# Kernel optimization log

Measured on AMD Instinct MI355X. Metric: run time of the kernel, lower is better.

The kernel has to match this reference:

```python
import jax, jax.numpy as jnp
import numpy as np

B, T, C = 4, 2048, 1024
H = 16
D = C // H  # head_dim = 64
SCALE = D ** -0.5


def setup_inputs() -> dict:
    key = jax.random.key(0)
    ks = jax.random.split(key, 5)
    x = jax.random.normal(ks[0], (B, T, C), dtype=jnp.float32)
    w_qkv = jax.random.normal(ks[1], (3 * C, C), dtype=jnp.float32) * (C ** -0.5)
    b_qkv = jnp.zeros((3 * C,), dtype=jnp.float32)
    w_proj = jax.random.normal(ks[2], (C, C), dtype=jnp.float32) * (C ** -0.5)
    b_proj = jnp.zeros((C,), dtype=jnp.float32)
    return {"x": x, "w_qkv": w_qkv, "b_qkv": b_qkv, "w_proj": w_proj, "b_proj": b_proj}


def reference(x, w_qkv, b_qkv, w_proj, b_proj):
    b, t, c = x.shape
    # fused qkv projection (torch Linear: x @ W.T + b)
    qkv = x @ w_qkv.T + b_qkv                      # [B, T, 3C]
    q, k, v = jnp.split(qkv, 3, axis=2)
    # [B, T, C] -> [B, H, T, D]
    q = q.reshape(b, t, H, D).transpose(0, 2, 1, 3)
    k = k.reshape(b, t, H, D).transpose(0, 2, 1, 3)
    v = v.reshape(b, t, H, D).transpose(0, 2, 1, 3)
    att = jnp.einsum('bhqd,bhkd->bhqk', q, k) * SCALE
    causal = jnp.tril(jnp.ones((t, t), dtype=bool))  # True = keep
    att = jnp.where(causal, att, -jnp.inf)
    att = jax.nn.softmax(att, axis=-1)
    out = jnp.einsum('bhqk,bhkd->bhqd', att, v)
    out = out.transpose(0, 2, 1, 3).reshape(b, t, c)
    return out @ w_proj.T + b_proj
```

## Files before the change

### kernel.cpp

```cpp
#include <hip/hip_runtime.h>

typedef unsigned short u16;
typedef __attribute__((ext_vector_type(8))) short short8;
typedef __attribute__((ext_vector_type(4))) float f32x4;
typedef __attribute__((ext_vector_type(16))) float f32x16;
typedef __attribute__((ext_vector_type(2))) unsigned uint2v;
typedef __attribute__((ext_vector_type(4))) unsigned u32x4;

#define AS1 __attribute__((address_space(1)))
#define AS3 __attribute__((address_space(3)))

constexpr int Bn = 4, Tn = 2048, Cn = 1024, Hn = 16, Dn = 64;
constexpr float SCL_LOG2E = 0.125f * 1.44269504088896f;

__device__ __forceinline__ u16 f2bf(float f) {
  union { float f; unsigned u; } v; v.f = f;
  unsigned r = v.u + 0x7FFFu + ((v.u >> 16) & 1u);
  return (u16)(r >> 16);
}

__device__ __forceinline__ unsigned cvtpk_bf16(float a, float b) {
  unsigned r;
  asm("v_cvt_pk_bf16_f32 %0, %1, %2" : "=v"(r) : "v"(a), "v"(b));
  return r;
}

__global__ void cast_f32_to_bf16(const float* __restrict__ in, u16* __restrict__ out, int n4) {
  int i = blockIdx.x * 256 + threadIdx.x;
  if (i >= n4) return;
  float4 v = ((const float4*)in)[i];
  ushort4 o;
  o.x = f2bf(v.x); o.y = f2bf(v.y); o.z = f2bf(v.z); o.w = f2bf(v.w);
  ((ushort4*)out)[i] = o;
}

template <typename OT>
__global__ __launch_bounds__(512) void gemm8(
    const u16* __restrict__ A, const u16* __restrict__ Bm,
    const float* __restrict__ bias, OT* __restrict__ C,
    int M, int N, int K, int nbn, int qcols, float qscale)
{
  __shared__ u16 As[2][128 * 64];
  __shared__ u16 Bs[2][128 * 64];

  const int tid = threadIdx.x;
  const int lane = tid & 63;
  const int w = tid >> 6;
  const int wm = w >> 2, wn = w & 3;
  const int l15 = lane & 15, lg = lane >> 4;

  const int nwg = gridDim.x;
  const int wg = (blockIdx.x & 7) * (nwg >> 3) + (blockIdx.x >> 3);
  const int m0 = (wg / nbn) * 128;
  const int n0 = (wg % nbn) * 128;
  const int NT = K >> 6;

  const int wrow = wm * 64;
  const int wcol = wn * 32;

  f32x4 acc[4][2] = {};

  auto stage_A = [&](int tt) {
    if (tt >= NT) return;
    const int bu = tt & 1;
#pragma unroll
    for (int it = 0; it < 2; ++it) {
      const int c = it * 512 + tid;
      const int row = c >> 3;
      const int cs = (c & 7) ^ (row & 7);
      const u16* g = A + (size_t)(m0 + row) * K + tt * 64 + cs * 8;
      __builtin_amdgcn_global_load_lds((const AS1 void*)g,
          (AS3 void*)(&As[bu][c * 8]), 16, 0, 0);
    }
  };
  auto stage_B = [&](int tt) {
    if (tt >= NT) return;
    const int bu = tt & 1;
#pragma unroll
    for (int it = 0; it < 2; ++it) {
      const int c = it * 512 + tid;
      const int row = c >> 3;
      const int cs = (c & 7) ^ (row & 7);
      const u16* g = Bm + (size_t)(n0 + row) * K + tt * 64 + cs * 8;
      __builtin_amdgcn_global_load_lds((const AS1 void*)g,
          (AS3 void*)(&Bs[bu][c * 8]), 16, 0, 0);
    }
  };

  auto readA = [&](int bu, int mh, short8 (*a)[2]) {
#pragma unroll
    for (int i = 0; i < 2; ++i)
#pragma unroll
      for (int ks = 0; ks < 2; ++ks) {
        const int ra = wrow + (mh * 2 + i) * 16 + l15;
        a[i][ks] = *(const short8*)(&As[bu][ra * 64 + (((ks * 4 + lg) ^ (ra & 7)) << 3)]);
      }
  };
  auto readB = [&](int bu, int nh, short8 (*b)[2]) {
#pragma unroll
    for (int ks = 0; ks < 2; ++ks) {
      const int rb = wcol + nh * 16 + l15;
      b[0][ks] = *(const short8*)(&Bs[bu][rb * 64 + (((ks * 4 + lg) ^ (rb & 7)) << 3)]);
    }
  };
  auto mmaq = [&](int mh, int nh, short8 (*a)[2], short8 (*b)[2]) {
    __builtin_amdgcn_s_setprio(1);
#pragma unroll
    for (int i = 0; i < 2; ++i)
#pragma unroll
      for (int ks = 0; ks < 2; ++ks)
        acc[mh * 2 + i][nh] = __builtin_amdgcn_mfma_f32_16x16x32_bf16(
            a[i][ks], b[0][ks], acc[mh * 2 + i][nh], 0, 0, 0);
    __builtin_amdgcn_s_setprio(0);
  };

  stage_A(0);
  stage_B(0);
  stage_A(1);
  asm volatile("s_waitcnt vmcnt(2)" ::: "memory");
  __builtin_amdgcn_sched_barrier(0);
  __builtin_amdgcn_s_barrier();

  for (int t = 0; t < NT; ++t) {
    const int bu = t & 1;
    short8 a0[2][2], a1[2][2], b0[1][2], b1[1][2];
    readA(bu, 0, a0);
    readB(bu, 0, b0);
    stage_B(t + 1);
    __builtin_amdgcn_s_barrier();
    mmaq(0, 0, a0, b0);
    __builtin_amdgcn_s_barrier();
    readB(bu, 1, b1);
    __builtin_amdgcn_s_barrier();
    mmaq(0, 1, a0, b1);
    __builtin_amdgcn_s_barrier();
    readA(bu, 1, a1);
    __builtin_amdgcn_s_barrier();
    mmaq(1, 1, a1, b1);
    __builtin_amdgcn_s_barrier();
    stage_A(t + 2);
    __builtin_amdgcn_s_barrier();
    mmaq(1, 0, a1, b0);
    if (t + 2 < NT) {
      asm volatile("s_waitcnt vmcnt(2)" ::: "memory");
      __builtin_amdgcn_sched_barrier(0);
    } else if (t + 1 < NT) {
      asm volatile("s_waitcnt vmcnt(0)" ::: "memory");
      __builtin_amdgcn_sched_barrier(0);
    }
    __builtin_amdgcn_s_barrier();
  }

  __syncthreads();
  if constexpr (__is_same(OT, u16)) {
    u16* bounce = &As[0][0];
#pragma unroll
    for (int i = 0; i < 4; ++i)
#pragma unroll
      for (int j = 0; j < 2; ++j) {
        const int colg = n0 + wcol + j * 16 + l15;
        const float sc = (colg < qcols) ? qscale : 1.0f;
        const float bv = bias[colg];
#pragma unroll
        for (int r = 0; r < 4; ++r)
          bounce[(wrow + i * 16 + lg * 4 + r) * 128 + wcol + j * 16 + l15] =
              f2bf((acc[i][j][r] + bv) * sc);
      }
    __syncthreads();
#pragma unroll
    for (int s = 0; s < 4; ++s) {
      const int u = s * 512 + tid;
      const int row = u >> 4, col = (u & 15) * 8;
      *(short8*)(C + (size_t)(m0 + row) * N + n0 + col) =
          *(const short8*)(&bounce[row * 128 + col]);
    }
  } else {
    float* bounce = (float*)&As[0][0];
#pragma unroll
    for (int cch = 0; cch < 2; ++cch) {
      if (wm == cch) {
#pragma unroll
        for (int i = 0; i < 4; ++i)
#pragma unroll
          for (int j = 0; j < 2; ++j) {
            const int colg = n0 + wcol + j * 16 + l15;
            const float bv = bias[colg];
#pragma unroll
            for (int r = 0; r < 4; ++r)
              bounce[(i * 16 + lg * 4 + r) * 128 + wcol + j * 16 + l15] =
                  acc[i][j][r] + bv;
          }
      }
      __syncthreads();
#pragma unroll
      for (int s = 0; s < 4; ++s) {
        const int u = s * 512 + tid;
        const int row = u >> 5, col = (u & 31) * 4;
        *(f32x4*)((float*)C + (size_t)(m0 + cch * 64 + row) * N + n0 + col) =
            *(const f32x4*)(&bounce[row * 128 + col]);
      }
      __syncthreads();
    }
  }
}

__global__ __launch_bounds__(256) void transpose_v(
    const u16* __restrict__ qkv, u16* __restrict__ vt)
{
  __shared__ u16 tile[64][72];
  const int bh = blockIdx.x >> 5;
  const int tt = blockIdx.x & 31;
  const int b = bh >> 4;
  const int h = bh & 15;
  const int tid = threadIdx.x;
  const int trow = tid >> 2;
  const int dseg = tid & 3;

  const u16* src = qkv + (size_t)(b * Tn + tt * 64 + trow) * (3 * Cn) + 2 * Cn + h * Dn + dseg * 16;
  short8 v0 = *(const short8*)src;
  short8 v1 = *(const short8*)(src + 8);
#pragma unroll
  for (int e = 0; e < 8; ++e) {
    tile[dseg * 16 + e][trow] = (u16)v0[e];
    tile[dseg * 16 + 8 + e][trow] = (u16)v1[e];
  }
  __syncthreads();

  const int drow = tid >> 2;
  const int tseg = tid & 3;
  u16* dst = vt + (size_t)(bh * Dn + drow) * Tn + tt * 64 + tseg * 16;
  *(short8*)dst = *(const short8*)&tile[drow][tseg * 16];
  *(short8*)(dst + 8) = *(const short8*)&tile[drow][tseg * 16 + 8];
}

__global__ __launch_bounds__(256) void attn_kernel(
    const u16* __restrict__ qkv, const u16* __restrict__ vt, u16* __restrict__ att)
{
  __shared__ u16 Ks[2][64 * 64];
  __shared__ u16 Vs[2][64 * 64];
  const int tid = threadIdx.x;
  const int lane = tid & 63;
  const int w = tid >> 6;
  const int l31 = lane & 31;
  const int hi = lane >> 5;

  const int blk = blockIdx.x;
  const int qt = (Tn / 128 - 1) - (blk >> 6);
  const int bh = blk & 63;
  const int b = bh >> 4;
  const int h = bh & 15;
  const int q0w = qt * 128 + w * 32;
  const int rowbase = b * Tn;
  const int koff = Cn + h * Dn;
  const size_t vbase = (size_t)bh * Dn * Tn;
  const int nt = 2 * qt + 2;
  const int ntw = 2 * qt + 1 + (w >> 1);

  short8 qf[4];
  {
    const u16* qp = qkv + (size_t)(rowbase + q0w + l31) * (3 * Cn) + h * Dn + hi * 8;
#pragma unroll
    for (int sub = 0; sub < 4; ++sub) qf[sub] = *(const short8*)(qp + sub * 16);
  }

  float m_r = -1e30f, l_r = 0.f;
  f32x16 oacc[2] = {};

#define STAGE(buf, t_)                                                            \
  {                                                                               \
    const int kt_ = (t_) * 64;                                                    \
    _Pragma("unroll")                                                             \
    for (int it = 0; it < 2; ++it) {                                              \
      int c = it * 256 + tid;                                                     \
      int row = c >> 3;                                                           \
      int cs = (c & 7) ^ (row & 7);                                               \
      const u16* gk = qkv + (size_t)(rowbase + kt_ + row) * (3 * Cn) + koff + cs * 8; \
      __builtin_amdgcn_global_load_lds((const AS1 void*)gk, (AS3 void*)(&Ks[buf][c * 8]), 16, 0, 0); \
      const u16* gv = vt + vbase + (size_t)row * Tn + kt_ + cs * 8;               \
      __builtin_amdgcn_global_load_lds((const AS1 void*)gv, (AS3 void*)(&Vs[buf][c * 8]), 16, 0, 0); \
    }                                                                             \
  }

  STAGE(0, 0);
  __syncthreads();

  for (int t = 0; t < nt; ++t) {
    const int cur = t & 1;
    if (t + 1 < nt) STAGE(cur ^ 1, t + 1);
    if (t < ntw) {
      const int kt = t * 64;
      const u16* Kb = Ks[cur];
      const u16* Vb = Vs[cur];

      f32x16 s0 = {}, s1 = {};
#pragma unroll
      for (int sub = 0; sub < 4; ++sub) {
        const int ch = sub * 2 + hi;
        const int r0 = l31;
        short8 kf0 = *(const short8*)(Kb + r0 * 64 + ((ch ^ (r0 & 7)) << 3));
        s0 = __builtin_amdgcn_mfma_f32_32x32x16_bf16(kf0, qf[sub], s0, 0, 0, 0);
        const int r1 = 32 + l31;
        short8 kf1 = *(const short8*)(Kb + r1 * 64 + ((ch ^ (r1 & 7)) << 3));
        s1 = __builtin_amdgcn_mfma_f32_32x32x16_bf16(kf1, qf[sub], s1, 0, 0, 0);
      }

      if (kt + 63 > q0w) {
        const int qa = q0w + l31;
#pragma unroll
        for (int r = 0; r < 16; ++r) {
          const int k0 = kt + ((r & 3) + 8 * (r >> 2)) + 4 * hi;
          if (k0 > qa) s0[r] = -1e30f;
          if (k0 + 32 > qa) s1[r] = -1e30f;
        }
      }

      float mx = s0[0];
#pragma unroll
      for (int r = 1; r < 16; ++r) mx = fmaxf(mx, s0[r]);
#pragma unroll
      for (int r = 0; r < 16; ++r) mx = fmaxf(mx, s1[r]);
      mx = fmaxf(mx, __shfl_xor(mx, 32));

      if (__any(mx > m_r + 8.f)) {
        const float mnew = fmaxf(m_r, mx);
        const float a = __builtin_amdgcn_exp2f(m_r - mnew);
        m_r = mnew;
        l_r *= a;
#pragma unroll
        for (int r = 0; r < 16; ++r) { oacc[0][r] *= a; oacc[1][r] *= a; }
      }

      float ps = 0.f;
#pragma unroll
      for (int r = 0; r < 16; ++r) {
        s0[r] = __builtin_amdgcn_exp2f(s0[r] - m_r); ps += s0[r];
        s1[r] = __builtin_amdgcn_exp2f(s1[r] - m_r); ps += s1[r];
      }
      ps += __shfl_xor(ps, 32);
      l_r += ps;

      short8 pfr[4];
#pragma unroll
      for (int ks = 0; ks < 4; ++ks) {
        const f32x16& sv = (ks < 2) ? s0 : s1;
        const int base = (ks & 1) * 8;
        unsigned a0 = cvtpk_bf16(sv[base + 0], sv[base + 1]);
        unsigned a1 = cvtpk_bf16(sv[base + 2], sv[base + 3]);
        unsigned b0 = cvtpk_bf16(sv[base + 4], sv[base + 5]);
        unsigned b1 = cvtpk_bf16(sv[base + 6], sv[base + 7]);
        uint2v s_0 = __builtin_amdgcn_permlane32_swap(a0, b0, false, false);
        uint2v s_1 = __builtin_amdgcn_permlane32_swap(a1, b1, false, false);
        union { u32x4 u; short8 s; } cvt;
        cvt.u = (u32x4){s_0.x, s_1.x, s_0.y, s_1.y};
        pfr[ks] = cvt.s;
      }

#pragma unroll
      for (int j = 0; j < 2; ++j) {
        const int rv = j * 32 + l31;
        const int rsw = (rv & 7) << 3;
#pragma unroll
        for (int ks = 0; ks < 4; ++ks) {
          short8 vf = *(const short8*)(Vb + rv * 64 + (((ks * 2 + hi) << 3) ^ rsw));
          oacc[j] = __builtin_amdgcn_mfma_f32_32x32x16_bf16(vf, pfr[ks], oacc[j], 0, 0, 0);
        }
      }
    }
    __syncthreads();
  }

  {
    const float inv = __builtin_amdgcn_rcpf(l_r);
    u16* orow = att + (size_t)(rowbase + q0w + l31) * Cn + h * Dn + hi * 4;
#pragma unroll
    for (int j = 0; j < 2; ++j)
#pragma unroll
      for (int g = 0; g < 4; ++g) {
        ushort4 o;
#pragma unroll
        for (int c = 0; c < 4; ++c) o[c] = f2bf(oacc[j][g * 4 + c] * inv);
        *(ushort4*)(orow + j * 32 + g * 8) = o;
      }
  }
#undef STAGE
}

extern "C" void kernel_launch(void* const* d_in, const int* in_sizes, int n_in,
                              void* d_out, int out_size, void* d_ws, size_t ws_size,
                              hipStream_t stream) {
  const float* x      = (const float*)d_in[0];
  const float* w_qkv  = (const float*)d_in[1];
  const float* b_qkv  = (const float*)d_in[2];
  const float* w_proj = (const float*)d_in[3];
  const float* b_proj = (const float*)d_in[4];
  float* out = (float*)d_out;

  char* ws = (char*)d_ws;
  u16* x_bf     = (u16*)(ws);
  u16* wqkv_bf  = (u16*)(ws + 16777216);
  u16* wproj_bf = (u16*)(ws + 16777216 + 6291456);
  u16* qkv      = (u16*)(ws + 25165824);
  u16* att      = (u16*)(ws + 75497472);
  u16* vt       = x_bf;

  const int M = Bn * Tn;

  cast_f32_to_bf16<<<(M * Cn / 4 + 255) / 256, 256, 0, stream>>>(x, x_bf, M * Cn / 4);
  cast_f32_to_bf16<<<(3 * Cn * Cn / 4 + 255) / 256, 256, 0, stream>>>(w_qkv, wqkv_bf, 3 * Cn * Cn / 4);
  cast_f32_to_bf16<<<(Cn * Cn / 4 + 255) / 256, 256, 0, stream>>>(w_proj, wproj_bf, Cn * Cn / 4);

  gemm8<u16><<<1536, 512, 0, stream>>>(
      x_bf, wqkv_bf, b_qkv, qkv, M, 3 * Cn, Cn, 24, Cn, SCL_LOG2E);

  transpose_v<<<Bn * Hn * (Tn / 64), 256, 0, stream>>>(qkv, vt);

  attn_kernel<<<Bn * Hn * (Tn / 128), 256, 0, stream>>>(qkv, vt, att);

  gemm8<float><<<512, 512, 0, stream>>>(
      att, wproj_bf, b_proj, out, M, Cn, Cn, 8, 0, 1.0f);
}
```

Before: 174.5 us.

## Load K/V fragments directly from global into registers, drop LDS staging

Removes the shared-memory double-buffered K/V staging and block-wide barriers. Each wave now loads its own K and V MFMA fragments straight from global memory (relying on L1/L2 for reuse across the 4 waves), and iterates only over its own tile count. It also restructures the row max and sum reductions into tree form for more ILP. The trade is roughly 4x more global/L2 traffic for K/V and exposed load latency without software prefetch, in exchange for no LDS traffic or syncs.

```diff
diff --git a/kernel.cpp b/kernel.cpp
--- a/kernel.cpp
+++ b/kernel.cpp
@@ -236,8 +236,6 @@
 __global__ __launch_bounds__(256) void attn_kernel(
     const u16* __restrict__ qkv, const u16* __restrict__ vt, u16* __restrict__ att)
 {
-  __shared__ u16 Ks[2][64 * 64];
-  __shared__ u16 Vs[2][64 * 64];
   const int tid = threadIdx.x;
   const int lane = tid & 63;
   const int w = tid >> 6;
@@ -253,7 +251,6 @@
   const int rowbase = b * Tn;
   const int koff = Cn + h * Dn;
   const size_t vbase = (size_t)bh * Dn * Tn;
-  const int nt = 2 * qt + 2;
   const int ntw = 2 * qt + 1 + (w >> 1);
 
   short8 qf[4];
@@ -266,107 +263,98 @@
   float m_r = -1e30f, l_r = 0.f;
   f32x16 oacc[2] = {};
 
-#define STAGE(buf, t_)                                                            \
-  {                                                                               \
-    const int kt_ = (t_) * 64;                                                    \
-    _Pragma("unroll")                                                             \
-    for (int it = 0; it < 2; ++it) {                                              \
-      int c = it * 256 + tid;                                                     \
-      int row = c >> 3;                                                           \
-      int cs = (c & 7) ^ (row & 7);                                               \
-      const u16* gk = qkv + (size_t)(rowbase + kt_ + row) * (3 * Cn) + koff + cs * 8; \
-      __builtin_amdgcn_global_load_lds((const AS1 void*)gk, (AS3 void*)(&Ks[buf][c * 8]), 16, 0, 0); \
-      const u16* gv = vt + vbase + (size_t)row * Tn + kt_ + cs * 8;               \
-      __builtin_amdgcn_global_load_lds((const AS1 void*)gv, (AS3 void*)(&Vs[buf][c * 8]), 16, 0, 0); \
-    }                                                                             \
-  }
-
-  STAGE(0, 0);
-  __syncthreads();
-
-  for (int t = 0; t < nt; ++t) {
-    const int cur = t & 1;
-    if (t + 1 < nt) STAGE(cur ^ 1, t + 1);
-    if (t < ntw) {
-      const int kt = t * 64;
-      const u16* Kb = Ks[cur];
-      const u16* Vb = Vs[cur];
-
-      f32x16 s0 = {}, s1 = {};
+  for (int t = 0; t < ntw; ++t) {
+    const int kt = t * 64;
+
+    short8 kf0[4], kf1[4];
+    {
+      const u16* kp0 = qkv + (size_t)(rowbase + kt + l31) * (3 * Cn) + koff + hi * 8;
+      const u16* kp1 = kp0 + (size_t)32 * (3 * Cn);
 #pragma unroll
       for (int sub = 0; sub < 4; ++sub) {
-        const int ch = sub * 2 + hi;
-        const int r0 = l31;
-        short8 kf0 = *(const short8*)(Kb + r0 * 64 + ((ch ^ (r0 & 7)) << 3));
-        s0 = __builtin_amdgcn_mfma_f32_32x32x16_bf16(kf0, qf[sub], s0, 0, 0, 0);
-        const int r1 = 32 + l31;
-        short8 kf1 = *(const short8*)(Kb + r1 * 64 + ((ch ^ (r1 & 7)) << 3));
-        s1 = __builtin_amdgcn_mfma_f32_32x32x16_bf16(kf1, qf[sub], s1, 0, 0, 0);
-      }
-
-      if (kt + 63 > q0w) {
-        const int qa = q0w + l31;
-#pragma unroll
-        for (int r = 0; r < 16; ++r) {
-          const int k0 = kt + ((r & 3) + 8 * (r >> 2)) + 4 * hi;
-          if (k0 > qa) s0[r] = -1e30f;
-          if (k0 + 32 > qa) s1[r] = -1e30f;
-        }
-      }
-
-      float mx = s0[0];
-#pragma unroll
-      for (int r = 1; r < 16; ++r) mx = fmaxf(mx, s0[r]);
-#pragma unroll
-      for (int r = 0; r < 16; ++r) mx = fmaxf(mx, s1[r]);
-      mx = fmaxf(mx, __shfl_xor(mx, 32));
-
-      if (__any(mx > m_r + 8.f)) {
-        const float mnew = fmaxf(m_r, mx);
-        const float a = __builtin_amdgcn_exp2f(m_r - mnew);
-        m_r = mnew;
-        l_r *= a;
-#pragma unroll
-        for (int r = 0; r < 16; ++r) { oacc[0][r] *= a; oacc[1][r] *= a; }
-      }
-
-      float ps = 0.f;
+        kf0[sub] = *(const short8*)(kp0 + sub * 16);
+        kf1[sub] = *(const short8*)(kp1 + sub * 16);
+      }
+    }
+    short8 vf[2][4];
+#pragma unroll
+    for (int j = 0; j < 2; ++j) {
+      const u16* vp = vt + vbase + (size_t)(j * 32 + l31) * Tn + kt + hi * 8;
+#pragma unroll
+      for (int ks = 0; ks < 4; ++ks) vf[j][ks] = *(const short8*)(vp + ks * 16);
+    }
+
+    f32x16 s0 = {}, s1 = {};
+#pragma unroll
+    for (int sub = 0; sub < 4; ++sub) {
+      s0 = __builtin_amdgcn_mfma_f32_32x32x16_bf16(kf0[sub], qf[sub], s0, 0, 0, 0);
+      s1 = __builtin_amdgcn_mfma_f32_32x32x16_bf16(kf1[sub], qf[sub], s1, 0, 0, 0);
+    }
+
+    if (kt + 63 > q0w) {
+      const int qa = q0w + l31;
 #pragma unroll
       for (int r = 0; r < 16; ++r) {
-        s0[r] = __builtin_amdgcn_exp2f(s0[r] - m_r); ps += s0[r];
-        s1[r] = __builtin_amdgcn_exp2f(s1[r] - m_r); ps += s1[r];
-      }
-      ps += __shfl_xor(ps, 32);
-      l_r += ps;
-
-      short8 pfr[4];
-#pragma unroll
-      for (int ks = 0; ks < 4; ++ks) {
-        const f32x16& sv = (ks < 2) ? s0 : s1;
-        const int base = (ks & 1) * 8;
-        unsigned a0 = cvtpk_bf16(sv[base + 0], sv[base + 1]);
-        unsigned a1 = cvtpk_bf16(sv[base + 2], sv[base + 3]);
-        unsigned b0 = cvtpk_bf16(sv[base + 4], sv[base + 5]);
-        unsigned b1 = cvtpk_bf16(sv[base + 6], sv[base + 7]);
-        uint2v s_0 = __builtin_amdgcn_permlane32_swap(a0, b0, false, false);
-        uint2v s_1 = __builtin_amdgcn_permlane32_swap(a1, b1, false, false);
-        union { u32x4 u; short8 s; } cvt;
-        cvt.u = (u32x4){s_0.x, s_1.x, s_0.y, s_1.y};
-        pfr[ks] = cvt.s;
-      }
-
-#pragma unroll
-      for (int j = 0; j < 2; ++j) {
-        const int rv = j * 32 + l31;
-        const int rsw = (rv & 7) << 3;
-#pragma unroll
-        for (int ks = 0; ks < 4; ++ks) {
-          short8 vf = *(const short8*)(Vb + rv * 64 + (((ks * 2 + hi) << 3) ^ rsw));
-          oacc[j] = __builtin_amdgcn_mfma_f32_32x32x16_bf16(vf, pfr[ks], oacc[j], 0, 0, 0);
-        }
-      }
-    }
-    __syncthreads();
+        const int k0 = kt + ((r & 3) + 8 * (r >> 2)) + 4 * hi;
+        if (k0 > qa) s0[r] = -1e30f;
+        if (k0 + 32 > qa) s1[r] = -1e30f;
+      }
+    }
+
+    float tm[16];
+#pragma unroll
+    for (int r = 0; r < 16; ++r) tm[r] = fmaxf(s0[r], s1[r]);
+#pragma unroll
+    for (int st = 8; st >= 1; st >>= 1)
+#pragma unroll
+      for (int r = 0; r < st; ++r) tm[r] = fmaxf(tm[r], tm[r + st]);
+    float mx = fmaxf(tm[0], __shfl_xor(tm[0], 32));
+
+    if (__any(mx > m_r + 8.f)) {
+      const float mnew = fmaxf(m_r, mx);
+      const float a = __builtin_amdgcn_exp2f(m_r - mnew);
+      m_r = mnew;
+      l_r *= a;
+#pragma unroll
+      for (int r = 0; r < 16; ++r) { oacc[0][r] *= a; oacc[1][r] *= a; }
+    }
+
+    float ts[16];
+#pragma unroll
+    for (int r = 0; r < 16; ++r) {
+      s0[r] = __builtin_amdgcn_exp2f(s0[r] - m_r);
+      s1[r] = __builtin_amdgcn_exp2f(s1[r] - m_r);
+      ts[r] = s0[r] + s1[r];
+    }
+#pragma unroll
+    for (int st = 8; st >= 1; st >>= 1)
+#pragma unroll
+      for (int r = 0; r < st; ++r) ts[r] += ts[r + st];
+    float ps = ts[0];
+    ps += __shfl_xor(ps, 32);
+    l_r += ps;
+
+    short8 pfr[4];
+#pragma unroll
+    for (int ks = 0; ks < 4; ++ks) {
+      const f32x16& sv = (ks < 2) ? s0 : s1;
+      const int base = (ks & 1) * 8;
+      unsigned a0 = cvtpk_bf16(sv[base + 0], sv[base + 1]);
+      unsigned a1 = cvtpk_bf16(sv[base + 2], sv[base + 3]);
+      unsigned b0 = cvtpk_bf16(sv[base + 4], sv[base + 5]);
+      unsigned b1 = cvtpk_bf16(sv[base + 6], sv[base + 7]);
+      uint2v s_0 = __builtin_amdgcn_permlane32_swap(a0, b0, false, false);
+      uint2v s_1 = __builtin_amdgcn_permlane32_swap(a1, b1, false, false);
+      union { u32x4 u; short8 s; } cvt;
+      cvt.u = (u32x4){s_0.x, s_1.x, s_0.y, s_1.y};
+      pfr[ks] = cvt.s;
+    }
+
+#pragma unroll
+    for (int j = 0; j < 2; ++j)
+#pragma unroll
+      for (int ks = 0; ks < 4; ++ks)
+        oacc[j] = __builtin_amdgcn_mfma_f32_32x32x16_bf16(vf[j][ks], pfr[ks], oacc[j], 0, 0, 0);
   }
 
   {
@@ -382,7 +370,6 @@
         *(ushort4*)(orow + j * 32 + g * 8) = o;
       }
   }
-#undef STAGE
 }
 
 extern "C" void kernel_launch(void* const* d_in, const int* in_sizes, int n_in,
```

After: 250.3 us. 1.43x slower.
